# Optimization experiments

Hardware: AMD Instinct MI355X
Metric: run time of the kernel (lower is better)

Reference implementation:

```python
import jax, jax.numpy as jnp
import numpy as np

B, S, DIM = 2, 2048, 2048
H = 16
Q_RANK, KV_RANK = 512, 512
D_NOPE, D_ROPE, D_V = 128, 64, 128
D_QK = D_NOPE + D_ROPE  # 192
EPS = 1e-6
SCALE = D_QK ** -0.5


def setup_inputs() -> dict:
    key = jax.random.key(0)
    ks = jax.random.split(key, 8)
    x = jax.random.normal(ks[0], (B, S, DIM), dtype=jnp.float32)
    # real RoPE table: theta_i = 10000^{-2i/d}, angles = pos * theta
    inv_freq = 1.0 / (10000.0 ** (np.arange(0, D_ROPE, 2, dtype=np.float32) / D_ROPE))
    ang = np.arange(S, dtype=np.float32)[:, None] * inv_freq[None, :]  # (S, D_ROPE//2)
    freqs_cis = jnp.asarray(np.stack([np.cos(ang), np.sin(ang)], axis=-1))  # (S, 32, 2)
    std = 0.02
    wq_a = jax.random.normal(ks[1], (Q_RANK, DIM), dtype=jnp.float32) * std
    wq_b = jax.random.normal(ks[2], (H * D_QK, Q_RANK), dtype=jnp.float32) * std
    wkv_a = jax.random.normal(ks[3], (KV_RANK + D_ROPE, DIM), dtype=jnp.float32) * std
    wkv_b = jax.random.normal(ks[4], (H * (D_NOPE + D_V), KV_RANK), dtype=jnp.float32) * std
    wo = jax.random.normal(ks[5], (DIM, H * D_V), dtype=jnp.float32) * std
    q_norm_w = jnp.ones((Q_RANK,), dtype=jnp.float32)
    kv_norm_w = jnp.ones((KV_RANK,), dtype=jnp.float32)
    return {"x": x, "freqs_cis": freqs_cis, "wq_a": wq_a, "wq_b": wq_b,
            "q_norm_w": q_norm_w, "wkv_a": wkv_a, "kv_norm_w": kv_norm_w,
            "wkv_b": wkv_b, "wo": wo}


def _rmsnorm(x, w):
    var = jnp.mean(jnp.square(x), axis=-1, keepdims=True)
    return x * jax.lax.rsqrt(var + EPS) * w


def _rope(x, freqs_cis):
    # x: (B, S, h, d); freqs_cis: (S, d//2, 2) as (cos, sin). Pairs are interleaved (x0,x1),(x2,x3),...
    xr, xi = x[..., 0::2], x[..., 1::2]
    cos = freqs_cis[None, :, None, :, 0]
    sin = freqs_cis[None, :, None, :, 1]
    yr = xr * cos - xi * sin
    yi = xr * sin + xi * cos
    return jnp.stack([yr, yi], axis=-1).reshape(x.shape)


def reference(x, freqs_cis, wq_a, wq_b, q_norm_w, wkv_a, kv_norm_w, wkv_b, wo):
    b, s, _ = x.shape
    # low-rank Q projection: wq_a -> RMSNorm -> wq_b
    q = _rmsnorm(x @ wq_a.T, q_norm_w) @ wq_b.T
    q = q.reshape(b, s, H, D_QK)
    q_nope, q_pe = q[..., :D_NOPE], q[..., D_NOPE:]
    q = jnp.concatenate([q_nope, _rope(q_pe, freqs_cis)], axis=-1)  # (b,s,H,192)
    # KV path
    kv = x @ wkv_a.T  # (b,s,KV_RANK+D_ROPE)
    kv_lat, k_pe = kv[..., :KV_RANK], kv[..., KV_RANK:]
    k_pe = _rope(k_pe[:, :, None, :], freqs_cis)  # (b,s,1,64)
    kv = (_rmsnorm(kv_lat, kv_norm_w) @ wkv_b.T).reshape(b, s, H, D_NOPE + D_V)
    k_nope, v = kv[..., :D_NOPE], kv[..., D_NOPE:]
    k = jnp.concatenate([k_nope, jnp.broadcast_to(k_pe, (b, s, H, D_ROPE))], axis=-1)
    # causal scaled-dot-product attention
    scores = jnp.einsum('bshd,bthd->bhst', q, k) * SCALE
    mask = jnp.tril(jnp.ones((s, s), dtype=bool))
    scores = jnp.where(mask[None, None], scores, jnp.finfo(scores.dtype).min)
    probs = jax.nn.softmax(scores, axis=-1)
    out = jnp.einsum('bhst,bthd->bshd', probs, v).reshape(b, s, H * D_V)
    return out @ wo.T
```

## Files before the change

### kernel.cpp

```cpp
#include <hip/hip_runtime.h>
#include <cstdint>
#include <cstddef>


typedef unsigned short u16;
typedef unsigned int u32;
typedef unsigned long long u64;
typedef __attribute__((ext_vector_type(8))) short bf16x8;
typedef __attribute__((ext_vector_type(4))) float floatx4;

#define MFMA16x16x32 __builtin_amdgcn_mfma_f32_16x16x32_bf16

#define QSCALE 0.10411755f
#define THR_L2 11.541560f

__device__ __forceinline__ u16 f2bf(float f) {
  u32 u = __float_as_uint(f);
  u32 r = (u + 0x7fffu + ((u >> 16) & 1u)) >> 16;
  return (u16)r;
}
__device__ __forceinline__ float bf2f(u16 b) {
  return __uint_as_float(((u32)b) << 16);
}
__device__ __forceinline__ u32 cvtpk(float lo, float hi) {
  u32 r;
  asm("v_cvt_pk_bf16_f32 %0, %1, %2" : "=v"(r) : "v"(lo), "v"(hi));
  return r;
}
__device__ __forceinline__ void gload16(const void* g, void* l) {
  __builtin_amdgcn_global_load_lds(
      (const __attribute__((address_space(1))) void*)g,
      (__attribute__((address_space(3))) void*)l, 16, 0, 0);
}

__global__ __launch_bounds__(256) void cvt_all(
    const float* __restrict__ s0, const float* __restrict__ s1,
    const float* __restrict__ s2, const float* __restrict__ s3,
    const float* __restrict__ s4, const float* __restrict__ s5,
    u16* __restrict__ d0, u16* __restrict__ d1, u16* __restrict__ d2,
    u16* __restrict__ d3, u16* __restrict__ d4, u16* __restrict__ d5) {
  constexpr int ST1 = 2097152;
  constexpr int ST2 = ST1 + 262144;
  constexpr int ST3 = ST2 + 294912;
  constexpr int ST4 = ST3 + 393216;
  constexpr int ST5 = ST4 + 524288;
  constexpr int TOT = ST5 + 1048576;
  int i = blockIdx.x * 256 + threadIdx.x;
  int stride = gridDim.x * 256;
  for (; i < TOT; i += stride) {
    const float* sp;
    u16* dp;
    int j;
    if (i < ST1)      { sp = s0; dp = d0; j = i; }
    else if (i < ST2) { sp = s1; dp = d1; j = i - ST1; }
    else if (i < ST3) { sp = s2; dp = d2; j = i - ST2; }
    else if (i < ST4) { sp = s3; dp = d3; j = i - ST3; }
    else if (i < ST5) { sp = s4; dp = d4; j = i - ST4; }
    else              { sp = s5; dp = d5; j = i - ST5; }
    float4 v = ((const float4*)sp)[j];
    ushort4 o;
    o.x = f2bf(v.x); o.y = f2bf(v.y); o.z = f2bf(v.z); o.w = f2bf(v.w);
    ((ushort4*)dp)[j] = o;
  }
}

template <int BM, int BN, int EPI>
__global__ __launch_bounds__(512) void gemm8(const u16* __restrict__ A,
                                             const u16* __restrict__ B,
                                             void* __restrict__ Cv,
                                             int M, int N, int K,
                                             const float* __restrict__ fcp,
                                             void* __restrict__ aux) {
  constexpr int WM = BM / 2;
  constexpr int AF = WM / 16;
  constexpr int LA = BM * 4 / 512;
  constexpr int LB = BN * 4 / 512;
  constexpr int S = LA + LB;
  __shared__ alignas(16) u16 As[2][BM * 32];
  __shared__ alignas(16) u16 Bs[2][BN * 32];
  const int m0 = blockIdx.y * BM, n0 = blockIdx.x * BN;
  const int t = threadIdx.x;
  const int wv = t >> 6, lane = t & 63, g = lane >> 4, qq = lane & 15;
  const int wr = wv >> 2, wc = wv & 3;
  const int fsw = (qq >> 1) & 3;
  size_t aoff[LA], boff[LB];
#pragma unroll
  for (int i = 0; i < LA; ++i) {
    int seg = t + i * 512;
    int row = seg >> 2, sl = seg & 3;
    aoff[i] = (size_t)(m0 + row) * K + (sl ^ ((row >> 1) & 3)) * 8;
  }
#pragma unroll
  for (int i = 0; i < LB; ++i) {
    int seg = t + i * 512;
    int row = seg >> 2, sl = seg & 3;
    boff[i] = (size_t)(n0 + row) * K + (sl ^ ((row >> 1) & 3)) * 8;
  }
  const floatx4 fz = {0.f, 0.f, 0.f, 0.f};
  floatx4 acc[AF][4];
#pragma unroll
  for (int m = 0; m < AF; ++m)
#pragma unroll
    for (int n = 0; n < 4; ++n) acc[m][n] = fz;

#define GS8(buf, k0)                                                          \
  {                                                                           \
    _Pragma("unroll") for (int i = 0; i < LA; ++i)                            \
        gload16(&A[aoff[i] + (k0)], &As[buf][(size_t)(wv * 64 + i * 512) * 8]); \
    _Pragma("unroll") for (int i = 0; i < LB; ++i)                            \
        gload16(&B[boff[i] + (k0)], &Bs[buf][(size_t)(wv * 64 + i * 512) * 8]); \
  }

  const int nk = K >> 5;
  GS8(0, 0);
  GS8(1, 32);
  for (int kt = 0; kt < nk; ++kt) {
    asm volatile("" ::: "memory");
    if (kt + 1 < nk) {
      if constexpr (S == 4)
        asm volatile("s_waitcnt vmcnt(4)" ::: "memory");
      else
        asm volatile("s_waitcnt vmcnt(3)" ::: "memory");
    } else {
      asm volatile("s_waitcnt vmcnt(0)" ::: "memory");
    }
    __builtin_amdgcn_s_barrier();
    asm volatile("" ::: "memory");
    const u16* Ab = &As[kt & 1][0];
    const u16* Bb = &Bs[kt & 1][0];
    bf16x8 af[AF], bfr[4];
#pragma unroll
    for (int m = 0; m < AF; ++m)
      af[m] = *(const bf16x8*)&Ab[(wr * WM + m * 16 + qq) * 32 + ((g ^ fsw) * 8)];
#pragma unroll
    for (int n = 0; n < 4; ++n)
      bfr[n] = *(const bf16x8*)&Bb[(wc * 64 + n * 16 + qq) * 32 + ((g ^ fsw) * 8)];
    asm volatile("s_waitcnt lgkmcnt(0)" ::: "memory");
    __builtin_amdgcn_s_barrier();
    asm volatile("" ::: "memory");
    if (kt + 2 < nk) GS8(kt & 1, (kt + 2) * 32);
    __builtin_amdgcn_s_setprio(1);
#pragma unroll
    for (int m = 0; m < AF; ++m)
#pragma unroll
      for (int n = 0; n < 4; ++n)
        acc[m][n] = MFMA16x16x32(af[m], bfr[n], acc[m][n], 0, 0, 0);
    __builtin_amdgcn_s_setprio(0);
  }
#undef GS8

#pragma unroll
  for (int m = 0; m < AF; ++m)
#pragma unroll
    for (int n = 0; n < 4; ++n) {
      const int col16 = n0 + wc * 64 + n * 16;
      if constexpr (EPI == 0 || EPI == 1) {
#pragma unroll
        for (int r = 0; r < 4; ++r) {
          int row = m0 + wr * WM + m * 16 + 4 * g + r;
          int col = col16 + qq;
          if constexpr (EPI == 1)
            ((u16*)Cv)[(size_t)row * N + col] = f2bf(acc[m][n][r]);
          else
            ((float*)Cv)[(size_t)row * N + col] = acc[m][n][r];
        }
      } else if constexpr (EPI == 2) {
        const int h = col16 / 192;
        const int jb = col16 - h * 192 + qq;
#pragma unroll
        for (int r = 0; r < 4; ++r) {
          int row = m0 + wr * WM + m * 16 + 4 * g + r;
          int b = row >> 11, s = row & 2047;
          float own = acc[m][n][r];
          float par = __shfl_xor(own, 1);
          if ((qq & 1) == 0) {
            u32 w;
            if (jb < 128) {
              w = cvtpk(own * QSCALE, par * QSCALE);
            } else {
              int jp = (jb - 128) >> 1;
              float c = fcp[(s * 32 + jp) * 2];
              float sn = fcp[(s * 32 + jp) * 2 + 1];
              w = cvtpk((own * c - par * sn) * QSCALE,
                        (own * sn + par * c) * QSCALE);
            }
            *(u32*)((u16*)Cv + ((size_t)(b * 16 + h) * 2048 + s) * 192 + jb) = w;
          }
        }
      } else {
        const int h = col16 >> 8;
        const int jb = (col16 & 255) + qq;
        if (jb < 128) {
#pragma unroll
          for (int r = 0; r < 4; ++r) {
            int row = m0 + wr * WM + m * 16 + 4 * g + r;
            int b = row >> 11, s = row & 2047;
            float own = acc[m][n][r];
            float par = __shfl_xor(own, 1);
            if ((qq & 1) == 0)
              *(u32*)((u16*)Cv + ((size_t)(b * 16 + h) * 2048 + s) * 192 + jb) =
                  cvtpk(own, par);
          }
        } else {
          int row0 = m0 + wr * WM + m * 16 + 4 * g;
          int b = row0 >> 11, s0v = row0 & 2047;
          int dv = jb - 128;
          u32 lo = cvtpk(acc[m][n][0], acc[m][n][1]);
          u32 hi = cvtpk(acc[m][n][2], acc[m][n][3]);
          u64 w = (u64)lo | ((u64)hi << 32);
          *(u64*)((u16*)aux + ((size_t)(b * 16 + h) * 128 + dv) * 2048 + s0v) = w;
        }
      }
    }
}

__global__ __launch_bounds__(256) void rmsnorm_u16(const u16* __restrict__ in,
                                                   int stride,
                                                   const float* __restrict__ w,
                                                   u16* __restrict__ out) {
  const int row = blockIdx.x, t = threadIdx.x;
  __shared__ float wsum[4];
  u32 wv2 = *(const u32*)&in[(size_t)row * stride + 2 * t];
  float vx = bf2f((u16)wv2), vy = bf2f((u16)(wv2 >> 16));
  float ss = vx * vx + vy * vy;
#pragma unroll
  for (int off = 1; off < 64; off <<= 1) ss += __shfl_xor(ss, off);
  if ((t & 63) == 0) wsum[t >> 6] = ss;
  __syncthreads();
  float tot = wsum[0] + wsum[1] + wsum[2] + wsum[3];
  float r = rsqrtf(tot * (1.f / 512.f) + 1e-6f);
  *(u32*)&out[(size_t)row * 512 + 2 * t] =
      cvtpk(vx * r * w[2 * t], vy * r * w[2 * t + 1]);
}

__global__ __launch_bounds__(256) void rope_kpe_bcast(const u16* __restrict__ ap,
                                                      const float* __restrict__ fc,
                                                      u16* __restrict__ kbf) {
  int idx = blockIdx.x * 256 + threadIdx.x;
  int row = idx >> 5, j = idx & 31;
  int b = row >> 11, s = row & 2047;
  u32 wv2 = *(const u32*)&ap[(size_t)row * 1280 + 1024 + 2 * j];
  float xr = bf2f((u16)wv2), xi = bf2f((u16)(wv2 >> 16));
  float c = fc[(s * 32 + j) * 2], sn = fc[(s * 32 + j) * 2 + 1];
  u32 w = cvtpk(xr * c - xi * sn, xr * sn + xi * c);
#pragma unroll
  for (int h = 0; h < 16; ++h)
    *(u32*)&kbf[((size_t)(b * 16 + h) * 2048 + s) * 192 + 128 + 2 * j] = w;
}

__global__ __launch_bounds__(256, 4) void flash_attn(const u16* __restrict__ Q,
                                                     const u16* __restrict__ Kc,
                                                     const u16* __restrict__ VT,
                                                     u16* __restrict__ O) {
  __shared__ alignas(16) u16 Ks[2][32 * 192];
  __shared__ alignas(16) u16 Vs[2][128 * 32];
  const int bid = blockIdx.x;
  const int qt = 31 - (bid >> 5);
  const int bh = bid & 31;
  const int t = threadIdx.x, wv = t >> 6, lane = t & 63;
  const int g = lane >> 4, qq = lane & 15;
  const int qrow0 = qt * 64 + wv * 16;
  const int my_last = qrow0 + 15;
  const int q_glob = qrow0 + qq;
  const int nkt = 2 * qt + 2;

  int koffg[3], voffg[2];
#pragma unroll
  for (int i = 0; i < 3; ++i) {
    int seg = t + i * 256;
    int row = seg / 24, sl = seg - row * 24;
    koffg[i] = row * 192 + (sl ^ ((row >> 1) & 7)) * 8;
  }
#pragma unroll
  for (int i = 0; i < 2; ++i) {
    int seg = t + i * 256;
    int row = seg >> 2, sl = seg & 3;
    voffg[i] = row * 2048 + (sl ^ ((row >> 1) & 3)) * 8;
  }
  const u16* Kt0 = Kc + (size_t)bh * 2048 * 192;
  const u16* Vt0 = VT + (size_t)bh * 128 * 2048;

  bf16x8 qf[6];
  {
    const u16* qp = Q + ((size_t)bh * 2048 + qrow0 + qq) * 192;
#pragma unroll
    for (int kk = 0; kk < 6; ++kk) qf[kk] = *(const bf16x8*)&qp[kk * 32 + g * 8];
  }
  asm volatile("s_waitcnt vmcnt(0)" ::: "memory");

  const floatx4 fz = {0.f, 0.f, 0.f, 0.f};
  floatx4 oacc[8];
  floatx4 oacc_l = fz;
#pragma unroll
  for (int d = 0; d < 8; ++d) oacc[d] = fz;
  float m_run = -1e30f;

  bf16x8 ones;
#pragma unroll
  for (int i = 0; i < 8; ++i) ones[i] = (short)0x3f80;

  const int krow0 = 2 * qq;
  const int krow1 = 2 * qq + 1;
  const int xrk = qq & 7;
  const int vsw = (qq >> 1) & 3;

#define STAGE(buf, kt)                                                       \
  {                                                                          \
    const u16* Kg = Kt0 + (size_t)(kt) * (32 * 192);                         \
    const u16* Vg = Vt0 + (kt) * 32;                                         \
    _Pragma("unroll") for (int i = 0; i < 3; ++i)                            \
        gload16(Kg + koffg[i], &Ks[buf][(size_t)(wv * 64 + i * 256) * 8]);   \
    _Pragma("unroll") for (int i = 0; i < 2; ++i)                            \
        gload16(Vg + voffg[i], &Vs[buf][(size_t)(wv * 64 + i * 256) * 8]);   \
  }

  STAGE(0, 0);
  for (int kt = 0; kt < nkt; ++kt) {
    const int k0 = kt * 32;
    asm volatile("" ::: "memory");
    if (kt + 1 < nkt) {
      STAGE((kt + 1) & 1, kt + 1);
      asm volatile("s_waitcnt vmcnt(5)" ::: "memory");
    } else {
      asm volatile("s_waitcnt vmcnt(0)" ::: "memory");
    }
    __builtin_amdgcn_s_barrier();
    asm volatile("" ::: "memory");
    if (k0 <= my_last) {
      const u16* Kb = &Ks[kt & 1][0];
      const u16* Vb = &Vs[kt & 1][0];
      floatx4 s0 = fz, s1 = fz;
      __builtin_amdgcn_s_setprio(1);
#pragma unroll
      for (int kk = 0; kk < 6; ++kk) {
        int sl = kk * 4 + g;
        bf16x8 a0 = *(const bf16x8*)&Kb[krow0 * 192 + ((sl ^ xrk) * 8)];
        bf16x8 a1 = *(const bf16x8*)&Kb[krow1 * 192 + ((sl ^ xrk) * 8)];
        s0 = MFMA16x16x32(a0, qf[kk], s0, 0, 0, 0);
        s1 = MFMA16x16x32(a1, qf[kk], s1, 0, 0, 0);
      }
      __builtin_amdgcn_s_setprio(0);
      float v[8];
      if (k0 + 31 <= qrow0) {
#pragma unroll
        for (int r = 0; r < 4; ++r) {
          v[r] = s0[r];
          v[4 + r] = s1[r];
        }
      } else {
#pragma unroll
        for (int r = 0; r < 4; ++r) {
          int key0 = k0 + 8 * g + 2 * r;
          v[r] = (key0 <= q_glob) ? s0[r] : -1e30f;
          v[4 + r] = (key0 + 1 <= q_glob) ? s1[r] : -1e30f;
        }
      }
      float mloc = fmaxf(fmaxf(fmaxf(v[0], v[1]), fmaxf(v[2], v[3])),
                         fmaxf(fmaxf(v[4], v[5]), fmaxf(v[6], v[7])));
      if (!__all(mloc <= m_run + THR_L2)) {
        float mx = fmaxf(mloc, __shfl_xor(mloc, 16));
        mx = fmaxf(mx, __shfl_xor(mx, 32));
        float m_new = fmaxf(m_run, mx);
        float alpha = exp2f(m_run - m_new);
        m_run = m_new;
#pragma unroll
        for (int d = 0; d < 8; ++d)
#pragma unroll
          for (int r = 0; r < 4; ++r) oacc[d][r] *= alpha;
#pragma unroll
        for (int r = 0; r < 4; ++r) oacc_l[r] *= alpha;
      }
      float pex[8];
#pragma unroll
      for (int i = 0; i < 8; ++i) pex[i] = exp2f(v[i] - m_run);
      bf16x8 pf;
      ((u32*)&pf)[0] = cvtpk(pex[0], pex[4]);
      ((u32*)&pf)[1] = cvtpk(pex[1], pex[5]);
      ((u32*)&pf)[2] = cvtpk(pex[2], pex[6]);
      ((u32*)&pf)[3] = cvtpk(pex[3], pex[7]);
      __builtin_amdgcn_s_setprio(1);
#pragma unroll
      for (int d = 0; d < 8; ++d) {
        bf16x8 vf = *(const bf16x8*)&Vb[(d * 16 + qq) * 32 + ((g ^ vsw) * 8)];
        oacc[d] = MFMA16x16x32(vf, pf, oacc[d], 0, 0, 0);
      }
      oacc_l = MFMA16x16x32(ones, pf, oacc_l, 0, 0, 0);
      __builtin_amdgcn_s_setprio(0);
    }
    asm volatile("" ::: "memory");
    __builtin_amdgcn_s_barrier();
  }
#undef STAGE
  float linv = 1.f / oacc_l[0];
  const int b = bh >> 4, h = bh & 15;
  size_t rowoff = ((size_t)b * 2048 + qrow0 + qq) * 2048 + h * 128 + 4 * g;
#pragma unroll
  for (int d = 0; d < 8; ++d) {
    u32 lo = cvtpk(oacc[d][0] * linv, oacc[d][1] * linv);
    u32 hi = cvtpk(oacc[d][2] * linv, oacc[d][3] * linv);
    u64 w = (u64)lo | ((u64)hi << 32);
    *(u64*)&O[rowoff + d * 16] = w;
  }
}

extern "C" void kernel_launch(void* const* d_in, const int* in_sizes, int n_in,
                              void* d_out, int out_size, void* d_ws,
                              size_t ws_size, hipStream_t stream) {
  (void)in_sizes; (void)n_in; (void)out_size;
  const float* x = (const float*)d_in[0];
  const float* fc = (const float*)d_in[1];
  const float* wqa = (const float*)d_in[2];
  const float* wqb = (const float*)d_in[3];
  const float* qnw = (const float*)d_in[4];
  const float* wkva = (const float*)d_in[5];
  const float* kvnw = (const float*)d_in[6];
  const float* wkvb = (const float*)d_in[7];
  const float* wo = (const float*)d_in[8];
  float* out = (float*)d_out;
  char* ws = (char*)d_ws;

  size_t off = 0;
  auto alloc = [&](size_t bytes) {
    size_t o = off;
    off += (bytes + 255) & ~(size_t)255;
    return o;
  };
  const size_t o_xbf = alloc(16777216);
  const size_t o_wa = alloc(5242880);
  const size_t o_wqb = alloc(3145728);
  const size_t o_wkvb = alloc(4194304);
  const size_t o_wo = alloc(8388608);
  const size_t o_qln = alloc(4194304);
  const size_t o_kvln = alloc(4194304);
  const size_t o_ap = alloc(10485760);
  const size_t o_qbf = alloc(25165824);
  const size_t o_kbf = alloc(25165824);
  const size_t o_vt = alloc(16777216);
  if (ws_size < off) return;

  u16* xbf = (u16*)(ws + o_xbf);
  u16* wab = (u16*)(ws + o_wa);
  u16* wqbb = (u16*)(ws + o_wqb);
  u16* wkvbb = (u16*)(ws + o_wkvb);
  u16* wob = (u16*)(ws + o_wo);
  u16* qlatn = (u16*)(ws + o_qln);
  u16* kvlatn = (u16*)(ws + o_kvln);
  u16* ap = (u16*)(ws + o_ap);
  u16* qbf = (u16*)(ws + o_qbf);
  u16* kbf = (u16*)(ws + o_kbf);
  u16* vt = (u16*)(ws + o_vt);
  u16* attnbf = (u16*)(ws + o_xbf);

  cvt_all<<<2048, 256, 0, stream>>>(x, wqa, wkva, wqb, wkvb, wo,
                                    xbf, wab, wab + 1048576, wqbb, wkvbb, wob);

  gemm8<128, 256, 1><<<dim3(5, 32), 512, 0, stream>>>(
      xbf, wab, ap, 4096, 1280, 2048, nullptr, nullptr);
  rmsnorm_u16<<<4096, 256, 0, stream>>>(ap, 1280, qnw, qlatn);
  rmsnorm_u16<<<4096, 256, 0, stream>>>(ap + 512, 1280, kvnw, kvlatn);
  rope_kpe_bcast<<<512, 256, 0, stream>>>(ap, fc, kbf);

  gemm8<256, 256, 2><<<dim3(12, 16), 512, 0, stream>>>(
      qlatn, wqbb, qbf, 4096, 3072, 512, fc, nullptr);

  gemm8<256, 256, 3><<<dim3(16, 16), 512, 0, stream>>>(
      kvlatn, wkvbb, kbf, 4096, 4096, 512, nullptr, vt);

  flash_attn<<<1024, 256, 0, stream>>>(qbf, kbf, vt, attnbf);
  gemm8<128, 256, 0><<<dim3(8, 32), 512, 0, stream>>>(
      attnbf, wob, out, 4096, 2048, 2048, nullptr, nullptr);
}
```

Measured before the change: 288.2 us.

## Restructure GEMM into K=64 half-tile ping-pong schedule with interleaved loads

```diff
diff --git a/kernel.cpp b/kernel.cpp
--- a/kernel.cpp
+++ b/kernel.cpp
@@ -64,38 +64,41 @@
   }
 }
 
-template <int BM, int BN, int EPI>
-__global__ __launch_bounds__(512) void gemm8(const u16* __restrict__ A,
-                                             const u16* __restrict__ B,
-                                             void* __restrict__ Cv,
-                                             int M, int N, int K,
-                                             const float* __restrict__ fcp,
-                                             void* __restrict__ aux) {
+template <int BM, int EPI>
+__global__ __launch_bounds__(512) void gemm8p(const u16* __restrict__ A,
+                                              const u16* __restrict__ B,
+                                              void* __restrict__ Cv,
+                                              int M, int N, int K,
+                                              const float* __restrict__ fcp,
+                                              void* __restrict__ aux) {
   constexpr int WM = BM / 2;
   constexpr int AF = WM / 16;
-  constexpr int LA = BM * 4 / 512;
-  constexpr int LB = BN * 4 / 512;
-  constexpr int S = LA + LB;
-  __shared__ alignas(16) u16 As[2][BM * 32];
-  __shared__ alignas(16) u16 Bs[2][BN * 32];
-  const int m0 = blockIdx.y * BM, n0 = blockIdx.x * BN;
+  constexpr int AFH = AF / 2;
+  constexpr int HM = BM / 2;
+  constexpr int LAH = BM / 128;
+  __shared__ alignas(16) u16 Ah[2][2][HM * 64];
+  __shared__ alignas(16) u16 Bh[2][2][128 * 64];
+  const int m0 = blockIdx.y * BM, n0 = blockIdx.x * 256;
   const int t = threadIdx.x;
   const int wv = t >> 6, lane = t & 63, g = lane >> 4, qq = lane & 15;
   const int wr = wv >> 2, wc = wv & 3;
-  const int fsw = (qq >> 1) & 3;
-  size_t aoff[LA], boff[LB];
-#pragma unroll
-  for (int i = 0; i < LA; ++i) {
-    int seg = t + i * 512;
-    int row = seg >> 2, sl = seg & 3;
-    aoff[i] = (size_t)(m0 + row) * K + (sl ^ ((row >> 1) & 3)) * 8;
-  }
-#pragma unroll
-  for (int i = 0; i < LB; ++i) {
-    int seg = t + i * 512;
-    int row = seg >> 2, sl = seg & 3;
-    boff[i] = (size_t)(n0 + row) * K + (sl ^ ((row >> 1) & 3)) * 8;
-  }
+  const int xq = qq & 7;
+  const int brow0 = (wc & 1) * 64;
+  const int bhalf = wc >> 1;
+
+  size_t aoff[LAH];
+#pragma unroll
+  for (int i = 0; i < LAH; ++i) {
+    int seg = t + i * 512, row = seg >> 3, sl = seg & 7;
+    aoff[i] = (size_t)(m0 + row) * K + (sl ^ (row & 7)) * 8;
+  }
+  size_t boff[2];
+#pragma unroll
+  for (int i = 0; i < 2; ++i) {
+    int seg = t + i * 512, row = seg >> 3, sl = seg & 7;
+    boff[i] = (size_t)(n0 + row) * K + (sl ^ (row & 7)) * 8;
+  }
+
   const floatx4 fz = {0.f, 0.f, 0.f, 0.f};
   floatx4 acc[AF][4];
 #pragma unroll
@@ -103,51 +106,123 @@
 #pragma unroll
     for (int n = 0; n < 4; ++n) acc[m][n] = fz;
 
-#define GS8(buf, k0)                                                          \
-  {                                                                           \
-    _Pragma("unroll") for (int i = 0; i < LA; ++i)                            \
-        gload16(&A[aoff[i] + (k0)], &As[buf][(size_t)(wv * 64 + i * 512) * 8]); \
-    _Pragma("unroll") for (int i = 0; i < LB; ++i)                            \
-        gload16(&B[boff[i] + (k0)], &Bs[buf][(size_t)(wv * 64 + i * 512) * 8]); \
-  }
-
-  const int nk = K >> 5;
-  GS8(0, 0);
-  GS8(1, 32);
-  for (int kt = 0; kt < nk; ++kt) {
-    asm volatile("" ::: "memory");
-    if (kt + 1 < nk) {
-      if constexpr (S == 4)
-        asm volatile("s_waitcnt vmcnt(4)" ::: "memory");
-      else
-        asm volatile("s_waitcnt vmcnt(3)" ::: "memory");
-    } else {
-      asm volatile("s_waitcnt vmcnt(0)" ::: "memory");
+#define SAH(dd, h, kt)                                                        \
+  { _Pragma("unroll") for (int i = 0; i < LAH; ++i)                           \
+      gload16(A + aoff[i] + (size_t)(h) * HM * K + (size_t)(kt) * 64,         \
+              &Ah[dd][h][(wv * 64 + i * 512) * 8]); }
+#define SBH(dd, h, kt)                                                        \
+  { _Pragma("unroll") for (int i = 0; i < 2; ++i)                             \
+      gload16(B + boff[i] + (size_t)(h) * 128 * K + (size_t)(kt) * 64,        \
+              &Bh[dd][h][(wv * 64 + i * 512) * 8]); }
+#define FENCE asm volatile("" ::: "memory")
+#define BAR __builtin_amdgcn_s_barrier()
+#define LGKM0 asm volatile("s_waitcnt lgkmcnt(0)" ::: "memory")
+
+  const int NT = K >> 6;
+  SAH(0, 0, 0) SAH(0, 1, 0) SBH(0, 0, 0) SBH(0, 1, 0)
+  SAH(1, 0, 1) SAH(1, 1, 1)
+  if (LAH == 2)
+    asm volatile("s_waitcnt vmcnt(4)" ::: "memory");
+  else
+    asm volatile("s_waitcnt vmcnt(2)" ::: "memory");
+  BAR;
+  FENCE;
+
+  for (int kt = 0; kt < NT; ++kt) {
+    const int d = kt & 1;
+    const u16* Ahb = &Ah[d][wr][0];
+    const u16* Bhb = &Bh[d][bhalf][0];
+    bf16x8 a[AFH][2], b0[2][2], b1[2][2];
+    if (kt + 1 < NT) SBH(d ^ 1, 0, kt + 1)
+#pragma unroll
+    for (int mf = 0; mf < AFH; ++mf)
+#pragma unroll
+      for (int ks = 0; ks < 2; ++ks)
+        a[mf][ks] = *(const bf16x8*)
+            &Ahb[(mf * 16 + qq) * 64 + (((ks * 4 + g) ^ xq) * 8)];
+#pragma unroll
+    for (int nf = 0; nf < 2; ++nf)
+#pragma unroll
+      for (int ks = 0; ks < 2; ++ks)
+        b0[nf][ks] = *(const bf16x8*)
+            &Bhb[(brow0 + nf * 16 + qq) * 64 + (((ks * 4 + g) ^ xq) * 8)];
+    FENCE; BAR; LGKM0;
+    __builtin_amdgcn_s_setprio(1);
+#pragma unroll
+    for (int mf = 0; mf < AFH; ++mf)
+#pragma unroll
+      for (int nf = 0; nf < 2; ++nf)
+#pragma unroll
+        for (int ks = 0; ks < 2; ++ks)
+          acc[mf][nf] = MFMA16x16x32(a[mf][ks], b0[nf][ks], acc[mf][nf], 0, 0, 0);
+    __builtin_amdgcn_s_setprio(0);
+    FENCE; BAR;
+    if (kt + 1 < NT) SBH(d ^ 1, 1, kt + 1)
+#pragma unroll
+    for (int nf = 0; nf < 2; ++nf)
+#pragma unroll
+      for (int ks = 0; ks < 2; ++ks)
+        b1[nf][ks] = *(const bf16x8*)
+            &Bhb[(brow0 + (2 + nf) * 16 + qq) * 64 + (((ks * 4 + g) ^ xq) * 8)];
+    FENCE; BAR; LGKM0;
+    __builtin_amdgcn_s_setprio(1);
+#pragma unroll
+    for (int mf = 0; mf < AFH; ++mf)
+#pragma unroll
+      for (int nf = 0; nf < 2; ++nf)
+#pragma unroll
+        for (int ks = 0; ks < 2; ++ks)
+          acc[mf][2 + nf] =
+              MFMA16x16x32(a[mf][ks], b1[nf][ks], acc[mf][2 + nf], 0, 0, 0);
+    __builtin_amdgcn_s_setprio(0);
+    FENCE; BAR;
+#pragma unroll
+    for (int mf = 0; mf < AFH; ++mf)
+#pragma unroll
+      for (int ks = 0; ks < 2; ++ks)
+        a[mf][ks] = *(const bf16x8*)
+            &Ahb[(WM / 2 + mf * 16 + qq) * 64 + (((ks * 4 + g) ^ xq) * 8)];
+    FENCE; BAR; LGKM0;
+    __builtin_amdgcn_s_setprio(1);
+#pragma unroll
+    for (int mf = 0; mf < AFH; ++mf)
+#pragma unroll
+      for (int nf = 0; nf < 2; ++nf)
+#pragma unroll
+        for (int ks = 0; ks < 2; ++ks)
+          acc[AFH + mf][nf] =
+              MFMA16x16x32(a[mf][ks], b0[nf][ks], acc[AFH + mf][nf], 0, 0, 0);
+    __builtin_amdgcn_s_setprio(0);
+    FENCE; BAR;
+    if (kt + 2 < NT) { SAH(d, 0, kt + 2) SAH(d, 1, kt + 2) }
+    FENCE; BAR;
+    __builtin_amdgcn_s_setprio(1);
+#pragma unroll
+    for (int mf = 0; mf < AFH; ++mf)
+#pragma unroll
+      for (int nf = 0; nf < 2; ++nf)
+#pragma unroll
+        for (int ks = 0; ks < 2; ++ks)
+          acc[AFH + mf][2 + nf] =
+              MFMA16x16x32(a[mf][ks], b1[nf][ks], acc[AFH + mf][2 + nf], 0, 0, 0);
+    __builtin_amdgcn_s_setprio(0);
+    if (kt + 1 < NT) {
+      if (kt + 2 < NT) {
+        if (LAH == 2)
+          asm volatile("s_waitcnt vmcnt(4)" ::: "memory");
+        else
+          asm volatile("s_waitcnt vmcnt(2)" ::: "memory");
+      } else {
+        asm volatile("s_waitcnt vmcnt(0)" ::: "memory");
+      }
     }
-    __builtin_amdgcn_s_barrier();
-    asm volatile("" ::: "memory");
-    const u16* Ab = &As[kt & 1][0];
-    const u16* Bb = &Bs[kt & 1][0];
-    bf16x8 af[AF], bfr[4];
-#pragma unroll
-    for (int m = 0; m < AF; ++m)
-      af[m] = *(const bf16x8*)&Ab[(wr * WM + m * 16 + qq) * 32 + ((g ^ fsw) * 8)];
-#pragma unroll
-    for (int n = 0; n < 4; ++n)
-      bfr[n] = *(const bf16x8*)&Bb[(wc * 64 + n * 16 + qq) * 32 + ((g ^ fsw) * 8)];
-    asm volatile("s_waitcnt lgkmcnt(0)" ::: "memory");
-    __builtin_amdgcn_s_barrier();
-    asm volatile("" ::: "memory");
-    if (kt + 2 < nk) GS8(kt & 1, (kt + 2) * 32);
-    __builtin_amdgcn_s_setprio(1);
-#pragma unroll
-    for (int m = 0; m < AF; ++m)
-#pragma unroll
-      for (int n = 0; n < 4; ++n)
-        acc[m][n] = MFMA16x16x32(af[m], bfr[n], acc[m][n], 0, 0, 0);
-    __builtin_amdgcn_s_setprio(0);
-  }
-#undef GS8
+    FENCE; BAR;
+  }
+#undef SAH
+#undef SBH
+#undef FENCE
+#undef BAR
+#undef LGKM0
 
 #pragma unroll
   for (int m = 0; m < AF; ++m)
@@ -454,19 +529,19 @@
   cvt_all<<<2048, 256, 0, stream>>>(x, wqa, wkva, wqb, wkvb, wo,
                                     xbf, wab, wab + 1048576, wqbb, wkvbb, wob);
 
-  gemm8<128, 256, 1><<<dim3(5, 32), 512, 0, stream>>>(
+  gemm8p<128, 1><<<dim3(5, 32), 512, 0, stream>>>(
       xbf, wab, ap, 4096, 1280, 2048, nullptr, nullptr);
   rmsnorm_u16<<<4096, 256, 0, stream>>>(ap, 1280, qnw, qlatn);
   rmsnorm_u16<<<4096, 256, 0, stream>>>(ap + 512, 1280, kvnw, kvlatn);
   rope_kpe_bcast<<<512, 256, 0, stream>>>(ap, fc, kbf);
 
-  gemm8<256, 256, 2><<<dim3(12, 16), 512, 0, stream>>>(
+  gemm8p<256, 2><<<dim3(12, 16), 512, 0, stream>>>(
       qlatn, wqbb, qbf, 4096, 3072, 512, fc, nullptr);
 
-  gemm8<256, 256, 3><<<dim3(16, 16), 512, 0, stream>>>(
+  gemm8p<256, 3><<<dim3(16, 16), 512, 0, stream>>>(
       kvlatn, wkvbb, kbf, 4096, 4096, 512, nullptr, vt);
 
   flash_attn<<<1024, 256, 0, stream>>>(qbf, kbf, vt, attnbf);
-  gemm8<128, 256, 0><<<dim3(8, 32), 512, 0, stream>>>(
+  gemm8p<128, 0><<<dim3(8, 32), 512, 0, stream>>>(
       attnbf, wob, out, 4096, 2048, 2048, nullptr, nullptr);
 }
```

New measurement: 316.7 us. 9.9% more time.
